# Kernel tuning notes

Hardware: AMD Instinct MI355X
Metric: run time of the kernel (lower is better)

## Reference

```python
import jax, jax.numpy as jnp
import numpy as np

B, S, D, H = 2, 2048, 768, 12
DK = D // H

def setup_inputs() -> dict:
    key = jax.random.key(0)
    ks = jax.random.split(key, 11)
    sc = 0.02
    inp = {
        'Q': jax.random.normal(ks[0], (B, S, D), jnp.float32),
        'K': jax.random.normal(ks[1], (B, S, D), jnp.float32),
        'V': jax.random.normal(ks[2], (B, S, D), jnp.float32),
        # causal mask, broadcastable over batch and heads (1 = keep, 0 = mask)
        'mask': jnp.tril(jnp.ones((S, S), jnp.int32))[None, None, :, :],
        'Wq': jax.random.normal(ks[3], (D, D), jnp.float32) * sc,
        'bq': jax.random.normal(ks[4], (D,), jnp.float32) * sc,
        'Wk': jax.random.normal(ks[5], (D, D), jnp.float32) * sc,
        'bk': jax.random.normal(ks[6], (D,), jnp.float32) * sc,
        'Wv': jax.random.normal(ks[7], (D, D), jnp.float32) * sc,
        'bv': jax.random.normal(ks[8], (D,), jnp.float32) * sc,
        'Wo': jax.random.normal(ks[9], (D, D), jnp.float32) * sc,
        'bo': jax.random.normal(ks[10], (D,), jnp.float32) * sc,
    }
    return inp

def _split_heads(x):
    # [B,S,D] -> [B,H,S,DK]
    return x.reshape(B, S, H, DK).transpose(0, 2, 1, 3)

def reference(Q, K, V, mask, Wq, bq, Wk, bk, Wv, bv, Wo, bo):
    # torch Linear: y = x @ W.T + b
    q = _split_heads(Q @ Wq.T + bq)
    k = _split_heads(K @ Wk.T + bk)
    v = _split_heads(V @ Wv.T + bv)
    scores = jnp.einsum('bhqd,bhkd->bhqk', q, k) / jnp.sqrt(jnp.float32(DK))
    scores = jnp.where(mask == 0, jnp.float32(-1e9), scores)
    attn = jax.nn.softmax(scores, axis=-1)
    out = jnp.einsum('bhqk,bhkd->bhqd', attn, v)  # [B,H,S,DK]
    out = out.transpose(0, 2, 1, 3).reshape(B, S, D)
    return out @ Wo.T + bo
```

## Files before the change

kernel.cpp:

```cpp
#include <hip/hip_runtime.h>
#include <hip/hip_bf16.h>

#define H_  12
#define S_  2048
#define D_  768
#define DK_ 64

typedef __bf16 bf16x8 __attribute__((ext_vector_type(8)));
typedef __bf16 bf16x4 __attribute__((ext_vector_type(4)));
typedef float  f32x4  __attribute__((ext_vector_type(4)));

#define QSCALE 0.1803368801111137f

__device__ inline float exp2_fast(float x) {
  return __builtin_amdgcn_exp2f(x);
}

__device__ inline f32x4 mfma_bf16(bf16x8 a, bf16x8 b, f32x4 c) {
  return __builtin_amdgcn_mfma_f32_16x16x32_bf16(a, b, c, 0, 0, 0);
}

__device__ inline void gload16(const void* g, void* l) {
  __builtin_amdgcn_global_load_lds(
      (const __attribute__((address_space(1))) void*)g,
      (__attribute__((address_space(3))) void*)l, 16, 0, 0);
}

__device__ inline bf16x8 cvt2bf16(f32x4 a, f32x4 b) {
  bf16x8 r;
  r[0] = (__bf16)a[0]; r[1] = (__bf16)a[1];
  r[2] = (__bf16)a[2]; r[3] = (__bf16)a[3];
  r[4] = (__bf16)b[0]; r[5] = (__bf16)b[1];
  r[6] = (__bf16)b[2]; r[7] = (__bf16)b[3];
  return r;
}

__global__ __launch_bounds__(256)
void conv_w(const float* __restrict__ Wq, const float* __restrict__ Wk,
            const float* __restrict__ Wv, const float* __restrict__ Wo,
            __hip_bfloat16* __restrict__ out)
{
  const int i8 = blockIdx.x * 256 + threadIdx.x;
  const int mat = i8 / 73728;
  const int off = (i8 - mat * 73728) * 8;
  const float* src = (mat == 0) ? Wq : (mat == 1) ? Wk : (mat == 2) ? Wv : Wo;
  f32x4 a = *(const f32x4*)(src + off);
  f32x4 b = *(const f32x4*)(src + off + 4);
  *(bf16x8*)(out + (size_t)mat * 589824 + off) = cvt2bf16(a, b);
}

__global__ __launch_bounds__(256, 3)
void qkv_proj(const float* __restrict__ Q, const float* __restrict__ K,
              const float* __restrict__ V,
              const __hip_bfloat16* __restrict__ Wb,
              const float* __restrict__ bq, const float* __restrict__ bk,
              const float* __restrict__ bv,
              __hip_bfloat16* __restrict__ q_ws,
              __hip_bfloat16* __restrict__ k_ws,
              __hip_bfloat16* __restrict__ vT_ws)
{
  __shared__ alignas(16) __hip_bfloat16 Ald[128 * 32];
  __shared__ alignas(16) __hip_bfloat16 Bld[128 * 32];

  const int z = blockIdx.z;
  const float* X    = (z == 0) ? Q  : (z == 1) ? K  : V;
  const float* bias = (z == 0) ? bq : (z == 1) ? bk : bv;
  const __hip_bfloat16* Wz = Wb + (size_t)z * 589824;
  __hip_bfloat16* out = (z == 0) ? q_ws : (z == 1) ? k_ws : vT_ws;
  const bool vmode = (z == 2);
  const float osc = (z == 0) ? QSCALE : 1.0f;

  const int t    = threadIdx.x;
  const int w    = t >> 6;
  const int lane = t & 63;
  const int l15  = lane & 15;
  const int quad = lane >> 4;
  const int m0 = blockIdx.x * 128;
  const int n0 = blockIdx.y * 128;
  const int wm = (w >> 1) * 64;
  const int wn = (w & 1) * 64;

  __hip_bfloat16* Xbuf = vmode ? Bld : Ald;
  __hip_bfloat16* Wbuf = vmode ? Ald : Bld;

  const f32x4 fzero = {0.f, 0.f, 0.f, 0.f};
  f32x4 acc[4][4];
#pragma unroll
  for (int i = 0; i < 4; ++i)
#pragma unroll
    for (int j = 0; j < 4; ++j) acc[i][j] = fzero;

  const int ar = t >> 2, ac = t & 3;
  const int sw = ac ^ ((ar >> 1) & 3);
  const float* As0 = X + (size_t)(m0 + ar) * D_ + ac * 8;
  const float* As1 = X + (size_t)(m0 + ar + 64) * D_ + ac * 8;
  __hip_bfloat16* Xw0 = &Xbuf[((ar)      * 4 + sw) * 8];
  __hip_bfloat16* Xw1 = &Xbuf[((ar + 64) * 4 + sw) * 8];

  const int bp = (t & 3) ^ (((t >> 2) >> 1) & 3);
  const __hip_bfloat16* Bs0 = Wz + (size_t)(n0 + (t >> 2)) * D_ + bp * 8;
  const __hip_bfloat16* Bs1 = Wz + (size_t)(n0 + (t >> 2) + 64) * D_ + bp * 8;
  __hip_bfloat16* Wd0 = &Wbuf[t * 8];
  __hip_bfloat16* Wd1 = &Wbuf[(t + 256) * 8];

  int agrn[4], bgrn[4];
#pragma unroll
  for (int i = 0; i < 4; ++i) {
    int row = wm + 16 * i + l15;
    agrn[i] = (row * 4 + (quad ^ ((row >> 1) & 3))) * 8;
    row = wn + 16 * i + l15;
    bgrn[i] = (row * 4 + (quad ^ ((row >> 1) & 3))) * 8;
  }

  f32x4 a00 = *(const f32x4*)As0, a01 = *(const f32x4*)(As0 + 4);
  f32x4 a10 = *(const f32x4*)As1, a11 = *(const f32x4*)(As1 + 4);

  for (int k0 = 0; k0 < D_; k0 += 32) {
    *(bf16x8*)Xw0 = cvt2bf16(a00, a01);
    *(bf16x8*)Xw1 = cvt2bf16(a10, a11);
    gload16(Bs0 + k0, Wd0);
    gload16(Bs1 + k0, Wd1);
    __syncthreads();

    const int kn = k0 + 32;
    if (kn < D_) {
      a00 = *(const f32x4*)(As0 + kn); a01 = *(const f32x4*)(As0 + kn + 4);
      a10 = *(const f32x4*)(As1 + kn); a11 = *(const f32x4*)(As1 + kn + 4);
    }

    bf16x8 af[4], bfr[4];
#pragma unroll
    for (int i = 0; i < 4; ++i) af[i]  = *(const bf16x8*)&Ald[agrn[i]];
#pragma unroll
    for (int j = 0; j < 4; ++j) bfr[j] = *(const bf16x8*)&Bld[bgrn[j]];
#pragma unroll
    for (int i = 0; i < 4; ++i)
#pragma unroll
      for (int j = 0; j < 4; ++j)
        acc[i][j] = mfma_bf16(af[i], bfr[j], acc[i][j]);
    __syncthreads();
  }

  if (!vmode) {
#pragma unroll
    for (int j = 0; j < 4; ++j) {
      const int n_g = n0 + wn + 16 * j + l15;
      const float bv = bias[n_g];
      const int hh = n_g >> 6, dk = n_g & (DK_ - 1);
#pragma unroll
      for (int i = 0; i < 4; ++i) {
        const int mbase = m0 + wm + 16 * i + quad * 4;
#pragma unroll
        for (int r = 0; r < 4; ++r) {
          const int m_g = mbase + r;
          const int bb = m_g >> 11, ss = m_g & (S_ - 1);
          const float vout = (acc[i][j][r] + bv) * osc;
          out[(((size_t)(bb * H_ + hh)) * S_ + ss) * DK_ + dk] =
              __float2bfloat16(vout);
        }
      }
    }
  } else {
#pragma unroll
    for (int i = 0; i < 4; ++i) {
      const int nbase = n0 + wm + 16 * i + quad * 4;
#pragma unroll
      for (int r = 0; r < 4; ++r) {
        const int n_g = nbase + r;
        const float bv = bias[n_g];
        const int hh = n_g >> 6, dk = n_g & (DK_ - 1);
#pragma unroll
        for (int j = 0; j < 4; ++j) {
          const int m_g = m0 + wn + 16 * j + l15;
          const int bb = m_g >> 11, ss = m_g & (S_ - 1);
          const int ssp = (ss & ~31) | (((ss >> 2) & 3) << 3) |
                          (((ss >> 4) & 1) << 2) | (ss & 3);
          out[(((size_t)(bb * H_ + hh)) * DK_ + dk) * S_ + ssp] =
              __float2bfloat16(acc[i][j][r] + bv);
        }
      }
    }
  }
}

__global__ __launch_bounds__(256, 4)
void o_proj(const __hip_bfloat16* __restrict__ Xb,
            const __hip_bfloat16* __restrict__ Wob,
            const float* __restrict__ bias,
            float* __restrict__ outf)
{
  __shared__ alignas(16) __hip_bfloat16 Ald[64 * 32];
  __shared__ alignas(16) __hip_bfloat16 Bld[128 * 32];

  const int t    = threadIdx.x;
  const int w    = t >> 6;
  const int lane = t & 63;
  const int l15  = lane & 15;
  const int quad = lane >> 4;
  const int m0 = blockIdx.x * 64;
  const int n0 = blockIdx.y * 128;
  const int wm = (w >> 1) * 32;
  const int wn = (w & 1) * 64;

  const f32x4 fzero = {0.f, 0.f, 0.f, 0.f};
  f32x4 acc[2][4];
#pragma unroll
  for (int i = 0; i < 2; ++i)
#pragma unroll
    for (int j = 0; j < 4; ++j) acc[i][j] = fzero;

  const int ap = (t & 3) ^ (((t >> 2) >> 1) & 3);
  const __hip_bfloat16* As  = Xb  + (size_t)(m0 + (t >> 2)) * D_ + ap * 8;
  const __hip_bfloat16* Bs0 = Wob + (size_t)(n0 + (t >> 2)) * D_ + ap * 8;
  const __hip_bfloat16* Bs1 = Wob + (size_t)(n0 + (t >> 2) + 64) * D_ + ap * 8;
  __hip_bfloat16* Ad  = &Ald[t * 8];
  __hip_bfloat16* Bd0 = &Bld[t * 8];
  __hip_bfloat16* Bd1 = &Bld[(t + 256) * 8];

  int agrn[2], bgrn[4];
#pragma unroll
  for (int i = 0; i < 2; ++i) {
    const int row = wm + 16 * i + l15;
    agrn[i] = (row * 4 + (quad ^ ((row >> 1) & 3))) * 8;
  }
#pragma unroll
  for (int j = 0; j < 4; ++j) {
    const int row = wn + 16 * j + l15;
    bgrn[j] = (row * 4 + (quad ^ ((row >> 1) & 3))) * 8;
  }

  for (int k0 = 0; k0 < D_; k0 += 32) {
    gload16(As + k0, Ad);
    gload16(Bs0 + k0, Bd0);
    gload16(Bs1 + k0, Bd1);
    __syncthreads();

    bf16x8 af[2], bfr[4];
#pragma unroll
    for (int i = 0; i < 2; ++i) af[i]  = *(const bf16x8*)&Ald[agrn[i]];
#pragma unroll
    for (int j = 0; j < 4; ++j) bfr[j] = *(const bf16x8*)&Bld[bgrn[j]];
#pragma unroll
    for (int i = 0; i < 2; ++i)
#pragma unroll
      for (int j = 0; j < 4; ++j)
        acc[i][j] = mfma_bf16(af[i], bfr[j], acc[i][j]);
    __syncthreads();
  }

#pragma unroll
  for (int j = 0; j < 4; ++j) {
    const int n_g = n0 + wn + 16 * j + l15;
    const float bv = bias[n_g];
#pragma unroll
    for (int i = 0; i < 2; ++i) {
      const int mbase = m0 + wm + 16 * i + quad * 4;
#pragma unroll
      for (int r = 0; r < 4; ++r)
        outf[(size_t)(mbase + r) * D_ + n_g] = acc[i][j][r] + bv;
    }
  }
}

__global__ __launch_bounds__(128, 2)
void flash_attn(const __hip_bfloat16* __restrict__ q_ws,
                const __hip_bfloat16* __restrict__ k_ws,
                const __hip_bfloat16* __restrict__ vT_ws,
                __hip_bfloat16* __restrict__ o_ws)
{
  __shared__ alignas(16) __hip_bfloat16 Kld[128][72];
  __shared__ alignas(16) __hip_bfloat16 Vld[64][136];

  const int t = threadIdx.x, w = t >> 6, lane = t & 63;
  const int l15 = lane & 15, quad = lane >> 4;

  const int id   = blockIdx.x;
  const int slot = id & 7;
  const int jj   = id >> 3;
  const int grp  = jj >> 5;
  const int bh   = slot + 8 * grp;
  const int x    = ((jj & 31) + 13 * grp) & 31;

  const int b = bh / H_, h = bh % H_;
  const int tLo = x, tHi = 63 - x;
  const int flip = x & 1;
  const int myTile = (w ^ flip) ? tHi : tLo;
  const int qg0 = myTile * 32 + l15;
  const int qg1 = qg0 + 16;
  const int myNkt = (myTile >> 2) + 1;
  const int nktT  = (tHi >> 2) + 1;
  const size_t hbase = (size_t)bh * S_ * DK_;
  const size_t vtb   = (size_t)bh * DK_ * S_;

  bf16x8 qf0[2], qf1[2];
#pragma unroll
  for (int kk = 0; kk < 2; ++kk) {
    qf0[kk] = *(const bf16x8*)(q_ws + hbase + (size_t)qg0 * DK_ + kk * 32 + quad * 8);
    qf1[kk] = *(const bf16x8*)(q_ws + hbase + (size_t)qg1 * DK_ + kk * 32 + quad * 8);
  }

  const f32x4 fzero = {0.f, 0.f, 0.f, 0.f};
  const f32x4 cinit = {-16.f, -16.f, -16.f, -16.f};
  bf16x8 ones;
#pragma unroll
  for (int i = 0; i < 8; ++i) ones[i] = (__bf16)1.0f;

  f32x4 accO0[4], accO1[4];
#pragma unroll
  for (int jd = 0; jd < 4; ++jd) { accO0[jd] = fzero; accO1[jd] = fzero; }
  f32x4 accL0 = fzero, accL1 = fzero;

  const int kr = t >> 3, kc = t & 7;
  const int vr = t >> 4, vc = t & 15;
  const __hip_bfloat16* Kbase = k_ws + hbase + (size_t)kr * DK_ + kc * 8;
  const __hip_bfloat16* Vbase = vT_ws + vtb + (size_t)vr * S_ + vc * 8;

  bf16x8 rK[8], rV[8];
#pragma unroll
  for (int it = 0; it < 8; ++it) {
    rK[it] = *(const bf16x8*)(Kbase + (size_t)(16 * it) * DK_);
    rV[it] = *(const bf16x8*)(Vbase + (size_t)(8 * it) * S_);
  }

  for (int kt = 0; kt < nktT; ++kt) {
#pragma unroll
    for (int it = 0; it < 8; ++it) {
      *(bf16x8*)&Kld[16 * it + kr][kc * 8] = rK[it];
      *(bf16x8*)&Vld[8 * it + vr][vc * 8] = rV[it];
    }
    __syncthreads();

    if (kt + 1 < nktT) {
      const int k0n = (kt + 1) * 128;
#pragma unroll
      for (int it = 0; it < 8; ++it) {
        rK[it] = *(const bf16x8*)(Kbase + (size_t)(k0n + 16 * it) * DK_);
        rV[it] = *(const bf16x8*)(Vbase + (size_t)(8 * it) * S_ + k0n);
      }
    }

    if (kt < myNkt) {
      const int k0 = kt * 128;
      const bool maskt = (kt == myNkt - 1);

      bf16x8 pB0[4], pB1[4];
      __builtin_amdgcn_s_setprio(1);
#pragma unroll
      for (int s = 0; s < 4; ++s) {
        bf16x8 kfa0 = *(const bf16x8*)&Kld[32 * s + l15][quad * 8];
        bf16x8 kfa1 = *(const bf16x8*)&Kld[32 * s + l15][32 + quad * 8];
        bf16x8 kfb0 = *(const bf16x8*)&Kld[32 * s + 16 + l15][quad * 8];
        bf16x8 kfb1 = *(const bf16x8*)&Kld[32 * s + 16 + l15][32 + quad * 8];
        f32x4 sa0 = mfma_bf16(kfa0, qf0[0], cinit);
        sa0 = mfma_bf16(kfa1, qf0[1], sa0);
        f32x4 sb0 = mfma_bf16(kfb0, qf0[0], cinit);
        sb0 = mfma_bf16(kfb1, qf0[1], sb0);
        f32x4 sa1 = mfma_bf16(kfa0, qf1[0], cinit);
        sa1 = mfma_bf16(kfa1, qf1[1], sa1);
        f32x4 sb1 = mfma_bf16(kfb0, qf1[0], cinit);
        sb1 = mfma_bf16(kfb1, qf1[1], sb1);

        if (maskt) {
#pragma unroll
          for (int r = 0; r < 4; ++r) {
            const int ka = k0 + 32 * s + quad * 4 + r;
            const int kb = ka + 16;
            if (ka > qg0) sa0[r] = -1.0e9f;
            if (kb > qg0) sb0[r] = -1.0e9f;
            if (ka > qg1) sa1[r] = -1.0e9f;
            if (kb > qg1) sb1[r] = -1.0e9f;
          }
        }
#pragma unroll
        for (int i = 0; i < 4; ++i) {
          pB0[s][i]     = (__bf16)exp2_fast(sa0[i]);
          pB0[s][4 + i] = (__bf16)exp2_fast(sb0[i]);
          pB1[s][i]     = (__bf16)exp2_fast(sa1[i]);
          pB1[s][4 + i] = (__bf16)exp2_fast(sb1[i]);
        }
      }

#pragma unroll
      for (int s = 0; s < 4; ++s) {
#pragma unroll
        for (int jd = 0; jd < 4; ++jd) {
          bf16x8 vf = *(const bf16x8*)&Vld[16 * jd + l15][32 * s + quad * 8];
          accO0[jd] = mfma_bf16(vf, pB0[s], accO0[jd]);
          accO1[jd] = mfma_bf16(vf, pB1[s], accO1[jd]);
        }
        accL0 = mfma_bf16(ones, pB0[s], accL0);
        accL1 = mfma_bf16(ones, pB1[s], accL1);
      }
      __builtin_amdgcn_s_setprio(0);
    }
    __syncthreads();
  }

  const float inv0 = 1.f / accL0[0];
  const float inv1 = 1.f / accL1[0];
#pragma unroll
  for (int jd = 0; jd < 4; ++jd) {
    bf16x4 ov0, ov1;
#pragma unroll
    for (int r = 0; r < 4; ++r) {
      ov0[r] = (__bf16)(accO0[jd][r] * inv0);
      ov1[r] = (__bf16)(accO1[jd][r] * inv1);
    }
    *(bf16x4*)(o_ws + ((size_t)b * S_ + qg0) * D_ + h * DK_ + 16 * jd + quad * 4) = ov0;
    *(bf16x4*)(o_ws + ((size_t)b * S_ + qg1) * D_ + h * DK_ + 16 * jd + quad * 4) = ov1;
  }
}

extern "C" void kernel_launch(void* const* d_in, const int* in_sizes, int n_in,
                              void* d_out, int out_size, void* d_ws, size_t ws_size,
                              hipStream_t stream) {
  (void)in_sizes; (void)n_in; (void)out_size; (void)ws_size;
  const float* Q  = (const float*)d_in[0];
  const float* K  = (const float*)d_in[1];
  const float* V  = (const float*)d_in[2];
  const float* Wq = (const float*)d_in[4];
  const float* bq = (const float*)d_in[5];
  const float* Wk = (const float*)d_in[6];
  const float* bk = (const float*)d_in[7];
  const float* Wv = (const float*)d_in[8];
  const float* bv = (const float*)d_in[9];
  const float* Wo = (const float*)d_in[10];
  const float* bo = (const float*)d_in[11];
  float* out = (float*)d_out;

  const size_t WEL = (size_t)4 * 589824;
  const size_t NEL = (size_t)2 * S_ * D_;
  __hip_bfloat16* wb    = (__hip_bfloat16*)d_ws;
  __hip_bfloat16* q_ws  = wb + WEL;
  __hip_bfloat16* k_ws  = q_ws  + NEL;
  __hip_bfloat16* vT_ws = k_ws  + NEL;
  __hip_bfloat16* o_ws  = vT_ws + NEL;

  conv_w<<<1152, 256, 0, stream>>>(Wq, Wk, Wv, Wo, wb);
  qkv_proj<<<dim3(32, 6, 3), 256, 0, stream>>>(Q, K, V, wb, bq, bk, bv,
                                               q_ws, k_ws, vT_ws);
  flash_attn<<<768, 128, 0, stream>>>(q_ws, k_ws, vT_ws, o_ws);
  o_proj<<<dim3(64, 6), 256, 0, stream>>>(o_ws, wb + (size_t)3 * 589824, bo, out);
}
```

Measured before the change: 188.9 us.

## Split KV tiles across paired waves in flash attention and merge partials

After: 253.4 us. 1.34x slower.

```diff
diff --git a/kernel.cpp b/kernel.cpp
--- a/kernel.cpp
+++ b/kernel.cpp
@@ -262,7 +262,7 @@
   }
 }
 
-__global__ __launch_bounds__(128, 2)
+__global__ __launch_bounds__(256, 3)
 void flash_attn(const __hip_bfloat16* __restrict__ q_ws,
                 const __hip_bfloat16* __restrict__ k_ws,
                 const __hip_bfloat16* __restrict__ vT_ws,
@@ -284,7 +284,8 @@
   const int b = bh / H_, h = bh % H_;
   const int tLo = x, tHi = 63 - x;
   const int flip = x & 1;
-  const int myTile = (w ^ flip) ? tHi : tLo;
+  const int myTile = ((w >> 1) ^ flip) ? tHi : tLo;
+  const int par = w & 1;
   const int qg0 = myTile * 32 + l15;
   const int qg1 = qg0 + 16;
   const int myNkt = (myTile >> 2) + 1;
@@ -310,36 +311,36 @@
   for (int jd = 0; jd < 4; ++jd) { accO0[jd] = fzero; accO1[jd] = fzero; }
   f32x4 accL0 = fzero, accL1 = fzero;
 
-  const int kr = t >> 3, kc = t & 7;
-  const int vr = t >> 4, vc = t & 15;
-  const __hip_bfloat16* Kbase = k_ws + hbase + (size_t)kr * DK_ + kc * 8;
-  const __hip_bfloat16* Vbase = vT_ws + vtb + (size_t)vr * S_ + vc * 8;
-
-  bf16x8 rK[8], rV[8];
-#pragma unroll
-  for (int it = 0; it < 8; ++it) {
-    rK[it] = *(const bf16x8*)(Kbase + (size_t)(16 * it) * DK_);
-    rV[it] = *(const bf16x8*)(Vbase + (size_t)(8 * it) * S_);
+  const int tr = t >> 3, kg = t & 7;
+  const int tv = t >> 4, vg = t & 15;
+  const __hip_bfloat16* Kbase = k_ws + hbase + (size_t)tr * DK_ + kg * 8;
+  const __hip_bfloat16* Vbase = vT_ws + vtb + (size_t)tv * S_ + vg * 8;
+
+  bf16x8 rK[4], rV[4];
+#pragma unroll
+  for (int it = 0; it < 4; ++it) {
+    rK[it] = *(const bf16x8*)(Kbase + (size_t)(32 * it) * DK_);
+    rV[it] = *(const bf16x8*)(Vbase + (size_t)(16 * it) * S_);
   }
 
   for (int kt = 0; kt < nktT; ++kt) {
 #pragma unroll
-    for (int it = 0; it < 8; ++it) {
-      *(bf16x8*)&Kld[16 * it + kr][kc * 8] = rK[it];
-      *(bf16x8*)&Vld[8 * it + vr][vc * 8] = rV[it];
+    for (int it = 0; it < 4; ++it) {
+      *(bf16x8*)&Kld[32 * it + tr][kg * 8] = rK[it];
+      *(bf16x8*)&Vld[16 * it + tv][vg * 8] = rV[it];
     }
     __syncthreads();
 
     if (kt + 1 < nktT) {
       const int k0n = (kt + 1) * 128;
 #pragma unroll
-      for (int it = 0; it < 8; ++it) {
-        rK[it] = *(const bf16x8*)(Kbase + (size_t)(k0n + 16 * it) * DK_);
-        rV[it] = *(const bf16x8*)(Vbase + (size_t)(8 * it) * S_ + k0n);
-      }
-    }
-
-    if (kt < myNkt) {
+      for (int it = 0; it < 4; ++it) {
+        rK[it] = *(const bf16x8*)(Kbase + (size_t)(k0n + 32 * it) * DK_);
+        rV[it] = *(const bf16x8*)(Vbase + (size_t)(16 * it) * S_ + k0n);
+      }
+    }
+
+    if (kt < myNkt && (kt & 1) == par) {
       const int k0 = kt * 128;
       const bool maskt = (kt == myNkt - 1);
 
@@ -396,18 +397,37 @@
     __syncthreads();
   }
 
-  const float inv0 = 1.f / accL0[0];
-  const float inv1 = 1.f / accL1[0];
-#pragma unroll
-  for (int jd = 0; jd < 4; ++jd) {
-    bf16x4 ov0, ov1;
-#pragma unroll
-    for (int r = 0; r < 4; ++r) {
-      ov0[r] = (__bf16)(accO0[jd][r] * inv0);
-      ov1[r] = (__bf16)(accO1[jd][r] * inv1);
-    }
-    *(bf16x4*)(o_ws + ((size_t)b * S_ + qg0) * D_ + h * DK_ + 16 * jd + quad * 4) = ov0;
-    *(bf16x4*)(o_ws + ((size_t)b * S_ + qg1) * D_ + h * DK_ + 16 * jd + quad * 4) = ov1;
+  float* cb = (float*)&Kld[0][0];
+  float* myc = cb + (((w >> 1) * 64 + lane) * 36);
+  if (par == 1) {
+#pragma unroll
+    for (int jd = 0; jd < 4; ++jd) {
+      *(f32x4*)(myc + 4 * jd)      = accO0[jd];
+      *(f32x4*)(myc + 16 + 4 * jd) = accO1[jd];
+    }
+    myc[32] = accL0[0];
+    myc[33] = accL1[0];
+  }
+  __syncthreads();
+  if (par == 0) {
+#pragma unroll
+    for (int jd = 0; jd < 4; ++jd) {
+      accO0[jd] += *(const f32x4*)(myc + 4 * jd);
+      accO1[jd] += *(const f32x4*)(myc + 16 + 4 * jd);
+    }
+    const float inv0 = 1.f / (accL0[0] + myc[32]);
+    const float inv1 = 1.f / (accL1[0] + myc[33]);
+#pragma unroll
+    for (int jd = 0; jd < 4; ++jd) {
+      bf16x4 ov0, ov1;
+#pragma unroll
+      for (int r = 0; r < 4; ++r) {
+        ov0[r] = (__bf16)(accO0[jd][r] * inv0);
+        ov1[r] = (__bf16)(accO1[jd][r] * inv1);
+      }
+      *(bf16x4*)(o_ws + ((size_t)b * S_ + qg0) * D_ + h * DK_ + 16 * jd + quad * 4) = ov0;
+      *(bf16x4*)(o_ws + ((size_t)b * S_ + qg1) * D_ + h * DK_ + 16 * jd + quad * 4) = ov1;
+    }
   }
 }
 
@@ -439,6 +459,6 @@
   conv_w<<<1152, 256, 0, stream>>>(Wq, Wk, Wv, Wo, wb);
   qkv_proj<<<dim3(32, 6, 3), 256, 0, stream>>>(Q, K, V, wb, bq, bk, bv,
                                                q_ws, k_ws, vT_ws);
-  flash_attn<<<768, 128, 0, stream>>>(q_ws, k_ws, vT_ws, o_ws);
+  flash_attn<<<768, 256, 0, stream>>>(q_ws, k_ws, vT_ws, o_ws);
   o_proj<<<dim3(64, 6), 256, 0, stream>>>(o_ws, wb + (size_t)3 * 589824, bo, out);
 }
```
